# Kernel tuning notes

Hardware: AMD Instinct MI355X
Metric: run time of the kernel (lower is better)

## Reference

```python
import jax, jax.numpy as jnp
import numpy as np

NUM_SLOTS = 8
SLOT_DIM = 3
WRITE_RATE = 0.1


def _amu(x, memory, Wk, bk, Ww, bw, Wg, bg, Wo, bo):
    """Associative Memory Unit.
    x: [B, T, Din], memory: [B, N, D] -> (outputs [B, T, Dout], memory [B, N, D]).
    Per step: softmax key-addressing read, gated erase/add write at WRITE_RATE,
    output = Linear(concat(x_t, read)).
    """
    xt = jnp.swapaxes(x, 0, 1)  # [T, B, Din]

    def step(mem, x_t):
        k = x_t @ Wk + bk                                   # [B, D]
        scores = jnp.einsum('bnd,bd->bn', mem, k)           # [B, N]
        w = jax.nn.softmax(scores, axis=-1)                 # addressing weights
        read = jnp.einsum('bn,bnd->bd', w, mem)             # [B, D]
        v = x_t @ Ww + bw                                   # write vector [B, D]
        e = jax.nn.sigmoid(x_t @ Wg + bg)                   # erase gate [B, D]
        we = w[:, :, None] * e[:, None, :]                  # [B, N, D]
        mem = mem * (1.0 - WRITE_RATE * we) + WRITE_RATE * w[:, :, None] * v[:, None, :]
        out = jnp.concatenate([x_t, read], axis=-1) @ Wo + bo
        return mem, out

    mem, outs = jax.lax.scan(step, memory, xt)
    return jnp.swapaxes(outs, 0, 1), mem


def setup_inputs() -> dict:
    key = jax.random.key(0)
    ks = jax.random.split(key, 12)
    B, T, D_in, D_hid, D_out = 64, 512, 128, 512, 128
    s = 0.05
    return {
        'inp': jax.random.normal(ks[0], (B, T, D_in), jnp.float32),
        'W1k': jax.random.normal(ks[1], (D_in, SLOT_DIM), jnp.float32) * s,
        'b1k': jnp.zeros((SLOT_DIM,), jnp.float32),
        'W1w': jax.random.normal(ks[2], (D_in, SLOT_DIM), jnp.float32) * s,
        'b1w': jnp.zeros((SLOT_DIM,), jnp.float32),
        'W1g': jax.random.normal(ks[3], (D_in, SLOT_DIM), jnp.float32) * s,
        'b1g': jnp.zeros((SLOT_DIM,), jnp.float32),
        'W1o': jax.random.normal(ks[4], (D_in + SLOT_DIM, D_hid), jnp.float32) * s,
        'b1o': jnp.zeros((D_hid,), jnp.float32),
        'W2k': jax.random.normal(ks[5], (D_hid, SLOT_DIM), jnp.float32) * s,
        'b2k': jnp.zeros((SLOT_DIM,), jnp.float32),
        'W2w': jax.random.normal(ks[6], (D_hid, SLOT_DIM), jnp.float32) * s,
        'b2w': jnp.zeros((SLOT_DIM,), jnp.float32),
        'W2g': jax.random.normal(ks[7], (D_hid, SLOT_DIM), jnp.float32) * s,
        'b2g': jnp.zeros((SLOT_DIM,), jnp.float32),
        'W2o': jax.random.normal(ks[8], (D_hid + SLOT_DIM, D_out), jnp.float32) * s,
        'b2o': jnp.zeros((D_out,), jnp.float32),
    }


def reference(inp, W1k, b1k, W1w, b1w, W1g, b1g, W1o, b1o,
              W2k, b2k, W2w, b2w, W2g, b2g, W2o, b2o):
    B = inp.shape[0]
    mem0 = jnp.zeros((B, NUM_SLOTS, SLOT_DIM), inp.dtype)
    o1, mem = _amu(inp, mem0, W1k, b1k, W1w, b1w, W1g, b1g, W1o, b1o)
    o1 = jax.nn.sigmoid(o1)  # self.layers = Sequential(Sigmoid())
    o2, mem = _amu(o1, mem, W2k, b2k, W2w, b2w, W2g, b2g, W2o, b2o)
    out = jax.nn.sigmoid(o2[:, -1, :])  # last timestep, then sigmoid
    return out
```

## Files before the change

kernel.cpp:

```cpp
#include <hip/hip_runtime.h>
#include <hip/hip_bf16.h>

#define B_ 64
#define T_ 512
#define LOG2E 1.4426950408889634f
#define PHASE_STEPS 16
#define NPHASE (T_/PHASE_STEPS)

typedef __attribute__((ext_vector_type(8))) short short8;
typedef __attribute__((ext_vector_type(4))) float f32x4;

__device__ __forceinline__ float fast_exp2(float x){ return __builtin_amdgcn_exp2f(x); }
__device__ __forceinline__ float fast_rcp(float x){ return __builtin_amdgcn_rcpf(x); }
__device__ __forceinline__ float sigmoidf_(float x){ return fast_rcp(1.0f + fast_exp2(-x*LOG2E)); }
__device__ __forceinline__ unsigned short f2bf(float f){
  union{float f; unsigned u;} v; v.f = f;
  unsigned r = v.u + 0x7fffu + ((v.u>>16)&1u);
  return (unsigned short)(r>>16);
}
template<typename T>
__device__ __forceinline__ void st_nt(T* p, T v){ __builtin_nontemporal_store(v, p); }

template<int CTRL>
__device__ __forceinline__ float dpp_xadd(float x){
  int y = __builtin_amdgcn_update_dpp(0, __float_as_int(x), CTRL, 0xf, 0xf, true);
  return x + __int_as_float(y);
}
__device__ __forceinline__ float dpp_sum8(float x){
  x = dpp_xadd<0xB1>(x);
  x = dpp_xadd<0x4E>(x);
  x = dpp_xadd<0x141>(x);
  return x;
}

__device__ __forceinline__ unsigned ld_rlx_u32(unsigned* p){
  return __hip_atomic_load(p, __ATOMIC_RELAXED, __HIP_MEMORY_SCOPE_AGENT);
}
__device__ __forceinline__ float ld_rlx_f32(const float* p){
  return __hip_atomic_load(p, __ATOMIC_RELAXED, __HIP_MEMORY_SCOPE_AGENT);
}
template<int SLP>
__device__ __forceinline__ void spin_rlx(unsigned* p, unsigned tgt){
  while (ld_rlx_u32(p) < tgt) __builtin_amdgcn_s_sleep(SLP);
  asm volatile("" ::: "memory");
}
__device__ __forceinline__ void acq_fence(){ __builtin_amdgcn_fence(__ATOMIC_ACQUIRE, "agent"); }
__device__ __forceinline__ void flag_add(unsigned* p){
  __builtin_amdgcn_fence(__ATOMIC_RELEASE, "agent");
  __hip_atomic_fetch_add(p, 1u, __ATOMIC_RELAXED, __HIP_MEMORY_SCOPE_AGENT);
}

template<int STORE_ALL, int IS_P1>
__device__ __forceinline__ void scan_role(const float* __restrict__ P,
    float* __restrict__ Rout, int bh,
    unsigned* cnt_in, unsigned tgt, unsigned* cnt_out, char* smemc)
{
  float (*buf)[PHASE_STEPS*288] = (float (*)[PHASE_STEPS*288])smemc;
  int tid = threadIdx.x;
  int wv = tid >> 6, lane = tid & 63;
  const float* Pb = P + bh*4608;
  if (wv == 4){
    #pragma unroll 1
    for (int p = 0; p < NPHASE; ++p){
      if (lane == 0) spin_rlx<1>(&cnt_in[p], tgt);
      asm volatile("" ::: "memory");
      const float* src = Pb + (long)p*9216;
      float tmp[72];
      #pragma unroll
      for (int i=0;i<18;++i){
        int u0 = 4*(lane + 64*i);
        #pragma unroll
        for (int k=0;k<4;++k) tmp[i*4+k] = ld_rlx_f32(src + u0 + k);
      }
      float* dst = buf[p&1];
      #pragma unroll
      for (int i=0;i<18;++i){
        #pragma unroll
        for (int k=0;k<4;++k){
          int u = 4*(lane + 64*i) + k;
          int bl, s, j;
          if (IS_P1){
            int q = u/576; int r = u - q*576; int row = r/9; j = r - row*9;
            bl = 4*q + (row>>4); s = row & 15;
          } else {
            int b2 = u/144; int r = u - b2*144; s = r/9; j = r - s*9; bl = b2;
          }
          dst[s*288 + j*32 + bl] = tmp[i*4+k];
        }
      }
      __syncthreads();
    }
    __syncthreads();
  } else {
    int g = lane >> 3, slot = lane & 7;
    int bl = wv*8 + g;
    int batch = bh*32 + bl;
    float m0=0.f, m1=0.f, m2=0.f;
    __syncthreads();
    #pragma unroll 1
    for (int p = 0; p < NPHASE; ++p){
      const float* bp = buf[p&1];
      float pp[3][9];
      #pragma unroll
      for (int j=0;j<9;++j){ pp[0][j] = bp[j*32+bl]; pp[1][j] = bp[288 + j*32+bl]; }
      #pragma unroll
      for (int s=0;s<PHASE_STEPS;++s){
        if (s+2 < PHASE_STEPS){
          #pragma unroll
          for (int j=0;j<9;++j) pp[(s+2)%3][j] = bp[(s+2)*288 + j*32 + bl];
        }
        const float* pv = pp[s%3];
        float sc = fmaf(m2, pv[2], fmaf(m1, pv[1], m0*pv[0]));
        float pe = fast_exp2(sc);
        float S = dpp_sum8(pe);
        float rinv = fast_rcp(S);
        float w = pe * rinv;
        if (STORE_ALL){
          float r0 = dpp_sum8(pe*m0);
          float r1 = dpp_sum8(pe*m1);
          float r2 = dpp_sum8(pe*m2);
          float rsel = (slot==0) ? r0 : ((slot==1) ? r1 : r2);
          rsel *= rinv;
          if (slot < 3) st_nt(&Rout[((p*PHASE_STEPS+s)*3 + slot)*64 + batch], rsel);
        } else if (s == PHASE_STEPS-1 && p == NPHASE-1){
          float r0 = dpp_sum8(pe*m0);
          float r1 = dpp_sum8(pe*m1);
          float r2 = dpp_sum8(pe*m2);
          float rsel = (slot==0) ? r0 : ((slot==1) ? r1 : r2);
          rsel *= rinv;
          if (slot < 3) st_nt(&Rout[slot*64 + batch], rsel);
        }
        float v0=pv[3], v1=pv[4], v2=pv[5], e0=pv[6], e1=pv[7], e2=pv[8];
        m0 = fmaf(w, fmaf(-e0, m0, v0), m0);
        m1 = fmaf(w, fmaf(-e1, m1, v1), m1);
        m2 = fmaf(w, fmaf(-e2, m2, v2), m2);
      }
      __syncthreads();
      if (cnt_out && tid == 0) flag_add(&cnt_out[p]);
    }
  }
}

__global__ __launch_bounds__(320,1) void k_mega(
    const float* __restrict__ X,
    const float* __restrict__ W1k, const float* __restrict__ b1k,
    const float* __restrict__ W1w, const float* __restrict__ b1w,
    const float* __restrict__ W1g, const float* __restrict__ b1g,
    const float* __restrict__ W1o, const float* __restrict__ b1o,
    const float* __restrict__ W2k, const float* __restrict__ b2k,
    const float* __restrict__ W2w, const float* __restrict__ b2w,
    const float* __restrict__ W2g, const float* __restrict__ b2g,
    float* __restrict__ P1, float* __restrict__ R1,
    float* __restrict__ P2, float* __restrict__ O1last, float* __restrict__ R2F,
    unsigned short* __restrict__ W1oTb, unsigned short* __restrict__ W2cTb,
    unsigned* __restrict__ flags)
{
  __shared__ __align__(16) char smem[40448];
  unsigned* proj_cnt  = flags;
  unsigned* r1_cnt    = flags + 32;
  unsigned* fused_cnt = flags + 64;
  unsigned* prep_cnt  = flags + 96;
  int role = blockIdx.x;
  int tid = threadIdx.x;

  if (role < 2){ scan_role<1,1>(P1, R1, role, proj_cnt, 16, r1_cnt, smem); return; }
  if (role < 4){ scan_role<0,0>(P2, R2F, role-2, fused_cnt, 64, nullptr, smem); return; }

  int wid = role - 4;
  int NW = (int)gridDim.x - 4;

  {
    int NT = NW*320;
    int gthread = wid*320 + tid;
    for (int x = gthread; x < 65536; x += NT){
      int n = x >> 7, k = x & 127;
      st_nt(&W1oTb[x], f2bf(W1o[k*512 + n]));
    }
    for (int x = gthread; x < 8192; x += NT){
      int j = x >> 9, cc = x & 511;
      float v = 0.f;
      if (j < 3) v = W2k[cc*3+j];
      else if (j < 6) v = W2w[cc*3+j-3];
      else if (j < 9) v = W2g[cc*3+j-6];
      st_nt(&W2cTb[x], f2bf(v));
    }
    __syncthreads();
    if (tid == 0) flag_add(prep_cnt);
  }

  {
    float* A  = (float*)smem;
    float* Wc = (float*)(smem + 33792);
    float* bb = (float*)(smem + 39936);
    for (int w_=tid; w_<1152; w_+=320){
      int k=w_/9, j=w_%9; float val;
      if (j<3) val=W1k[k*3+j]; else if (j<6) val=W1w[k*3+j-3]; else val=W1g[k*3+j-6];
      Wc[k*12+j]=val;
    }
    if (tid<9){ float v; if(tid<3)v=b1k[tid]; else if(tid<6)v=b1w[tid-3]; else v=b1g[tid-6]; bb[tid]=v; }
    __syncthreads();
    #pragma unroll 1
    for (int i = wid; i < 512; i += NW){
      int c = i >> 4, q = i & 15;
      if (tid < 256){
        #pragma unroll
        for (int it=0; it<8; ++it){
          int f4 = tid + it*256;
          int blk = f4 >> 9, off = f4 & 511;
          const float4* src = (const float4*)(X + ((long)(4*q+blk)*512 + 16*c)*128);
          float4 v = src[off];
          int f = off*4, trow = f>>7, k = f&127;
          int row = blk*16 + trow;
          A[row*132+k]=v.x; A[row*132+k+1]=v.y; A[row*132+k+2]=v.z; A[row*132+k+3]=v.w;
        }
      }
      __syncthreads();
      for (int o = tid; o < 576; o += 320){
        int row=o/9, j=o%9;
        float acc = bb[j];
        #pragma unroll 8
        for (int k=0;k<128;++k) acc = fmaf(A[row*132+k], Wc[k*12+j], acc);
        if (j<3) acc *= LOG2E;
        else if (j<6) acc *= 0.1f;
        else acc = 0.1f*sigmoidf_(acc);
        st_nt(&P1[(long)i*576 + o], acc);
      }
      __syncthreads();
      if (tid == 0) flag_add(&proj_cnt[c]);
    }
  }

  if (tid == 0) spin_rlx<8>(prep_cnt, (unsigned)NW);
  __syncthreads();
  acq_fence();

  {
    float* pSum = (float*)smem;
    float* rdS  = (float*)(smem + 4096);
    unsigned short* o1b = (unsigned short*)(smem + 4352);
    int w = tid >> 6, lane = tid & 63;
    int n16 = lane & 15, g4 = lane >> 4;
    #pragma unroll 1
    for (int i = wid; i < 2048; i += NW){
      int c = i >> 6, b = i & 63;
      if (tid == 0) spin_rlx<16>(&r1_cnt[c], 2);
      __syncthreads();
      int t0 = c*16;
      long r0 = (long)b*512 + t0;
      if (tid < 48){
        int ii = tid/3, d = tid%3;
        rdS[tid] = ld_rlx_f32(&R1[((t0+ii)*3+d)*64 + b]);
      }
      short8 afr[4];
      if (w < 4){
        const float* Xrow = X + (r0 + n16)*128;
        #pragma unroll
        for (int q=0;q<4;++q){
          f32x4 x0 = *(const f32x4*)(Xrow + q*32 + g4*8);
          f32x4 x1 = *(const f32x4*)(Xrow + q*32 + g4*8 + 4);
          short8 a;
          a[0]=(short)f2bf(x0[0]); a[1]=(short)f2bf(x0[1]);
          a[2]=(short)f2bf(x0[2]); a[3]=(short)f2bf(x0[3]);
          a[4]=(short)f2bf(x1[0]); a[5]=(short)f2bf(x1[1]);
          a[6]=(short)f2bf(x1[2]); a[7]=(short)f2bf(x1[3]);
          afr[q]=a;
        }
      }
      __syncthreads();
      if (w < 4){
        f32x4 ra = *(const f32x4*)(rdS + g4*12);
        f32x4 rb = *(const f32x4*)(rdS + g4*12 + 4);
        f32x4 rc = *(const f32x4*)(rdS + g4*12 + 8);
        float rd0[4] = { ra[0], ra[3], rb[2], rc[1] };
        float rd1[4] = { ra[1], rb[0], rb[3], rc[2] };
        float rd2[4] = { ra[2], rb[1], rc[0], rc[3] };
        #pragma unroll
        for (int tt=0; tt<8; ++tt){
          int gc = w*128 + tt*16 + n16;
          f32x4 acc = {0.f,0.f,0.f,0.f};
          #pragma unroll
          for (int q=0;q<4;++q){
            short8 bf = *(const short8*)(W1oTb + gc*128 + q*32 + g4*8);
            acc = __builtin_amdgcn_mfma_f32_16x16x32_bf16(afr[q], bf, acc, 0,0,0);
          }
          float bias = b1o[gc];
          float wr0 = W1o[128*512+gc], wr1 = W1o[129*512+gc], wr2 = W1o[130*512+gc];
          #pragma unroll
          for (int reg=0; reg<4; ++reg){
            int rowloc = g4*4 + reg;
            float z = acc[reg] + bias + rd0[reg]*wr0 + rd1[reg]*wr1 + rd2[reg]*wr2;
            float o1 = sigmoidf_(z);
            o1b[rowloc*520 + gc] = f2bf(o1);
            if (c == 31 && rowloc == 15) st_nt(&O1last[b*512 + gc], o1);
          }
        }
        f32x4 accP = {0.f,0.f,0.f,0.f};
        #pragma unroll
        for (int q2=0; q2<4; ++q2){
          int kk = w*128 + q2*32;
          short8 a2 = *(const short8*)(o1b + n16*520 + kk + g4*8);
          short8 bb2 = *(const short8*)(W2cTb + n16*512 + kk + g4*8);
          accP = __builtin_amdgcn_mfma_f32_16x16x32_bf16(a2, bb2, accP, 0,0,0);
        }
        #pragma unroll
        for (int reg=0;reg<4;++reg){
          int rowloc = g4*4+reg;
          pSum[w*256 + rowloc*16 + n16] = accP[reg];
        }
      }
      __syncthreads();
      if (tid < 144){
        int r = tid/9, j = tid%9;
        float s = pSum[r*16+j] + pSum[256+r*16+j] + pSum[512+r*16+j] + pSum[768+r*16+j];
        float outv;
        if (j<3){ s += b2k[j]; outv = s*LOG2E; }
        else if (j<6){ s += b2w[j-3]; outv = 0.1f*s; }
        else { s += b2g[j-6]; outv = 0.1f*sigmoidf_(s); }
        st_nt(&P2[(long)i*144 + tid], outv);
      }
      __syncthreads();
      if (tid == 0) flag_add(&fused_cnt[c]);
    }
  }
}

__global__ __launch_bounds__(128) void k_final(const float* __restrict__ O1last,
    const float* __restrict__ R2F, const float* __restrict__ W2o,
    const float* __restrict__ b2o, float* __restrict__ out)
{
  __shared__ __align__(16) float s2[512];
  int b = blockIdx.x, tid = threadIdx.x;
  ((float4*)s2)[tid] = ((const float4*)(O1last + b*512))[tid];
  __syncthreads();
  float acc = b2o[tid];
  #pragma unroll 8
  for (int n=0;n<512;++n) acc = fmaf(s2[n], W2o[n*128+tid], acc);
  float r0 = R2F[b], r1 = R2F[64+b], r2 = R2F[128+b];
  acc += r0*W2o[512*128+tid] + r1*W2o[513*128+tid] + r2*W2o[514*128+tid];
  out[b*128+tid] = sigmoidf_(acc);
}

extern "C" void kernel_launch(void* const* d_in, const int* in_sizes, int n_in,
                              void* d_out, int out_size, void* d_ws, size_t ws_size,
                              hipStream_t stream)
{
  const float* X  = (const float*)d_in[0];
  const float* W1k= (const float*)d_in[1]; const float* b1k=(const float*)d_in[2];
  const float* W1w= (const float*)d_in[3]; const float* b1w=(const float*)d_in[4];
  const float* W1g= (const float*)d_in[5]; const float* b1g=(const float*)d_in[6];
  const float* W1o= (const float*)d_in[7]; const float* b1o=(const float*)d_in[8];
  const float* W2k= (const float*)d_in[9]; const float* b2k=(const float*)d_in[10];
  const float* W2w= (const float*)d_in[11]; const float* b2w=(const float*)d_in[12];
  const float* W2g= (const float*)d_in[13]; const float* b2g=(const float*)d_in[14];
  const float* W2o= (const float*)d_in[15]; const float* b2o=(const float*)d_in[16];

  float* ws = (float*)d_ws;
  float* P1     = ws;
  float* R1     = P1 + 294912;
  float* P2     = R1 + 98304;
  float* O1last = P2 + 294912;
  float* R2F    = O1last + 32768;
  unsigned short* W1oTb = (unsigned short*)(R2F + 192);
  unsigned short* W2cTb = W1oTb + 65536;
  unsigned* flags = (unsigned*)(R2F + 192 + 32768 + 4096);
  float* out    = (float*)d_out;

  hipMemsetAsync(flags, 0, 512, stream);
  hipLaunchKernelGGL(k_mega, dim3(256), dim3(320), 0, stream,
                     X, W1k,b1k, W1w,b1w, W1g,b1g, W1o,b1o,
                     W2k,b2k, W2w,b2w, W2g,b2g,
                     P1, R1, P2, O1last, R2F, W1oTb, W2cTb, flags);
  hipLaunchKernelGGL(k_final, dim3(64), dim3(128), 0, stream,
                     O1last, R2F, W2o, b2o, out);
}
```

Measured before the change: 263.7 us.

## Pre-layout projection slabs for direct LDS copy and fuse final GEMV into mega kernel

Producers now write the P1/P2 projection slabs in the layout the scan consumer reads, with P2 rows padded to 152. The loader wave can then copy float4 chunks straight into LDS instead of scattering elements with div/mod index math. The separate k_final launch is removed. Instead, 64 worker blocks spin on a new scan2_done counter and compute the final output GEMV inside k_mega, saving one launch at the cost of those blocks waiting on the scan to finish.

```diff
diff --git a/kernel.cpp b/kernel.cpp
--- a/kernel.cpp
+++ b/kernel.cpp
@@ -55,38 +55,28 @@
     float* __restrict__ Rout, int bh,
     unsigned* cnt_in, unsigned tgt, unsigned* cnt_out, char* smemc)
 {
-  float (*buf)[PHASE_STEPS*288] = (float (*)[PHASE_STEPS*288])smemc;
+  const int NF4  = IS_P1 ? 18 : 19;
+  const int SLABF = IS_P1 ? 4608 : 4864;
+  const int PHS  = IS_P1 ? 9216 : 9728;
+  float* buf0 = (float*)smemc;
+  float* buf1 = buf0 + SLABF;
   int tid = threadIdx.x;
   int wv = tid >> 6, lane = tid & 63;
-  const float* Pb = P + bh*4608;
+  const float* Pb = P + bh*SLABF;
   if (wv == 4){
     #pragma unroll 1
     for (int p = 0; p < NPHASE; ++p){
       if (lane == 0) spin_rlx<1>(&cnt_in[p], tgt);
       asm volatile("" ::: "memory");
-      const float* src = Pb + (long)p*9216;
-      float tmp[72];
+      const float* src = Pb + (long)p*PHS;
+      float* dst = (p&1) ? buf1 : buf0;
       #pragma unroll
-      for (int i=0;i<18;++i){
+      for (int i=0;i<NF4;++i){
         int u0 = 4*(lane + 64*i);
-        #pragma unroll
-        for (int k=0;k<4;++k) tmp[i*4+k] = ld_rlx_f32(src + u0 + k);
-      }
-      float* dst = buf[p&1];
-      #pragma unroll
-      for (int i=0;i<18;++i){
-        #pragma unroll
-        for (int k=0;k<4;++k){
-          int u = 4*(lane + 64*i) + k;
-          int bl, s, j;
-          if (IS_P1){
-            int q = u/576; int r = u - q*576; int row = r/9; j = r - row*9;
-            bl = 4*q + (row>>4); s = row & 15;
-          } else {
-            int b2 = u/144; int r = u - b2*144; s = r/9; j = r - s*9; bl = b2;
-          }
-          dst[s*288 + j*32 + bl] = tmp[i*4+k];
-        }
+        f32x4 v;
+        v[0]=ld_rlx_f32(src+u0); v[1]=ld_rlx_f32(src+u0+1);
+        v[2]=ld_rlx_f32(src+u0+2); v[3]=ld_rlx_f32(src+u0+3);
+        *(f32x4*)(dst + u0) = v;
       }
       __syncthreads();
     }
@@ -95,19 +85,24 @@
     int g = lane >> 3, slot = lane & 7;
     int bl = wv*8 + g;
     int batch = bh*32 + bl;
+    int base = IS_P1 ? ((bl>>2)*576 + (bl&3)) : (bl*152);
     float m0=0.f, m1=0.f, m2=0.f;
     __syncthreads();
     #pragma unroll 1
     for (int p = 0; p < NPHASE; ++p){
-      const float* bp = buf[p&1];
+      const float* bp = ((p&1) ? buf1 : buf0) + base;
       float pp[3][9];
       #pragma unroll
-      for (int j=0;j<9;++j){ pp[0][j] = bp[j*32+bl]; pp[1][j] = bp[288 + j*32+bl]; }
+      for (int j=0;j<9;++j){
+        pp[0][j] = bp[IS_P1 ? j*4 : j];
+        pp[1][j] = bp[IS_P1 ? (9+j)*4 : (9+j)];
+      }
       #pragma unroll
       for (int s=0;s<PHASE_STEPS;++s){
         if (s+2 < PHASE_STEPS){
           #pragma unroll
-          for (int j=0;j<9;++j) pp[(s+2)%3][j] = bp[(s+2)*288 + j*32 + bl];
+          for (int j=0;j<9;++j)
+            pp[(s+2)%3][j] = bp[IS_P1 ? ((s+2)*9+j)*4 : ((s+2)*9+j)];
         }
         const float* pv = pp[s%3];
         float sc = fmaf(m2, pv[2], fmaf(m1, pv[1], m0*pv[0]));
@@ -150,21 +145,28 @@
     const float* __restrict__ W2k, const float* __restrict__ b2k,
     const float* __restrict__ W2w, const float* __restrict__ b2w,
     const float* __restrict__ W2g, const float* __restrict__ b2g,
+    const float* __restrict__ W2o, const float* __restrict__ b2o,
     float* __restrict__ P1, float* __restrict__ R1,
     float* __restrict__ P2, float* __restrict__ O1last, float* __restrict__ R2F,
     unsigned short* __restrict__ W1oTb, unsigned short* __restrict__ W2cTb,
-    unsigned* __restrict__ flags)
+    unsigned* __restrict__ flags, float* __restrict__ out)
 {
-  __shared__ __align__(16) char smem[40448];
+  __shared__ __align__(16) char smem[39936];
   unsigned* proj_cnt  = flags;
   unsigned* r1_cnt    = flags + 32;
   unsigned* fused_cnt = flags + 64;
   unsigned* prep_cnt  = flags + 96;
+  unsigned* scan2_done= flags + 97;
   int role = blockIdx.x;
   int tid = threadIdx.x;
 
   if (role < 2){ scan_role<1,1>(P1, R1, role, proj_cnt, 16, r1_cnt, smem); return; }
-  if (role < 4){ scan_role<0,0>(P2, R2F, role-2, fused_cnt, 64, nullptr, smem); return; }
+  if (role < 4){
+    scan_role<0,0>(P2, R2F, role-2, fused_cnt, 64, nullptr, smem);
+    __syncthreads();
+    if (tid == 0) flag_add(scan2_done);
+    return;
+  }
 
   int wid = role - 4;
   int NW = (int)gridDim.x - 4;
@@ -191,7 +193,7 @@
   {
     float* A  = (float*)smem;
     float* Wc = (float*)(smem + 33792);
-    float* bb = (float*)(smem + 39936);
+    float* bb = (float*)(smem + 39888);
     for (int w_=tid; w_<1152; w_+=320){
       int k=w_/9, j=w_%9; float val;
       if (j<3) val=W1k[k*3+j]; else if (j<6) val=W1w[k*3+j-3]; else val=W1g[k*3+j-6];
@@ -223,7 +225,7 @@
         if (j<3) acc *= LOG2E;
         else if (j<6) acc *= 0.1f;
         else acc = 0.1f*sigmoidf_(acc);
-        st_nt(&P1[(long)i*576 + o], acc);
+        st_nt(&P1[(long)i*576 + ((row&15)*9 + j)*4 + (row>>4)], acc);
       }
       __syncthreads();
       if (tid == 0) flag_add(&proj_cnt[c]);
@@ -316,28 +318,30 @@
         if (j<3){ s += b2k[j]; outv = s*LOG2E; }
         else if (j<6){ s += b2w[j-3]; outv = 0.1f*s; }
         else { s += b2g[j-6]; outv = 0.1f*sigmoidf_(s); }
-        st_nt(&P2[(long)i*144 + tid], outv);
+        st_nt(&P2[(long)i*152 + tid], outv);
       }
       __syncthreads();
       if (tid == 0) flag_add(&fused_cnt[c]);
     }
   }
-}
-
-__global__ __launch_bounds__(128) void k_final(const float* __restrict__ O1last,
-    const float* __restrict__ R2F, const float* __restrict__ W2o,
-    const float* __restrict__ b2o, float* __restrict__ out)
-{
-  __shared__ __align__(16) float s2[512];
-  int b = blockIdx.x, tid = threadIdx.x;
-  ((float4*)s2)[tid] = ((const float4*)(O1last + b*512))[tid];
-  __syncthreads();
-  float acc = b2o[tid];
-  #pragma unroll 8
-  for (int n=0;n<512;++n) acc = fmaf(s2[n], W2o[n*128+tid], acc);
-  float r0 = R2F[b], r1 = R2F[64+b], r2 = R2F[128+b];
-  acc += r0*W2o[512*128+tid] + r1*W2o[513*128+tid] + r2*W2o[514*128+tid];
-  out[b*128+tid] = sigmoidf_(acc);
+
+  if (wid < 64){
+    if (tid == 0) spin_rlx<16>(scan2_done, 2);
+    __syncthreads();
+    acq_fence();
+    float* s2 = (float*)smem;
+    if (tid < 128)
+      ((float4*)s2)[tid] = ((const float4*)(O1last + wid*512))[tid];
+    __syncthreads();
+    if (tid < 128){
+      float acc = b2o[tid];
+      #pragma unroll 8
+      for (int n=0;n<512;++n) acc = fmaf(s2[n], W2o[n*128+tid], acc);
+      float r0 = R2F[wid], r1 = R2F[64+wid], r2 = R2F[128+wid];
+      acc += r0*W2o[512*128+tid] + r1*W2o[513*128+tid] + r2*W2o[514*128+tid];
+      out[wid*128+tid] = sigmoidf_(acc);
+    }
+  }
 }
 
 extern "C" void kernel_launch(void* const* d_in, const int* in_sizes, int n_in,
@@ -358,7 +362,7 @@
   float* P1     = ws;
   float* R1     = P1 + 294912;
   float* P2     = R1 + 98304;
-  float* O1last = P2 + 294912;
+  float* O1last = P2 + 311296;
   float* R2F    = O1last + 32768;
   unsigned short* W1oTb = (unsigned short*)(R2F + 192);
   unsigned short* W2cTb = W1oTb + 65536;
@@ -368,8 +372,6 @@
   hipMemsetAsync(flags, 0, 512, stream);
   hipLaunchKernelGGL(k_mega, dim3(256), dim3(320), 0, stream,
                      X, W1k,b1k, W1w,b1w, W1g,b1g, W1o,b1o,
-                     W2k,b2k, W2w,b2w, W2g,b2g,
-                     P1, R1, P2, O1last, R2F, W1oTb, W2cTb, flags);
-  hipLaunchKernelGGL(k_final, dim3(64), dim3(128), 0, stream,
-                     O1last, R2F, W2o, b2o, out);
-}
+                     W2k,b2k, W2w,b2w, W2g,b2g, W2o,b2o,
+                     P1, R1, P2, O1last, R2F, W1oTb, W2cTb, flags, out);
+}
```

Result: slower. 471.6 us (+78.8%).
